# Kernel optimization log

Hardware: AMD Instinct MI355X
Metric: run time of the kernel (lower is better)

The kernel has to match this reference:

```python
import jax, jax.numpy as jnp
import numpy as np


def setup_inputs() -> dict:
    key = jax.random.key(0)
    k1, k2 = jax.random.split(key)
    K, D = 8192, 256
    z_e_x = jax.random.normal(k1, (4, D, 32, 64), dtype=jnp.float32)
    # matches uniform(-1/K, 1/K) init scale-wise, but any values work for correctness
    codebook = jax.random.uniform(k2, (K, D), dtype=jnp.float32, minval=-1.0 / K, maxval=1.0 / K)
    return {"z_e_x": z_e_x, "codebook": codebook}


def reference(z_e_x, codebook):
    b, D, h, t = z_e_x.shape
    K = codebook.shape[0]
    # permute to channels-last and flatten: [b*h*t, D]
    x = jnp.transpose(z_e_x, (0, 2, 3, 1)).reshape(-1, D)
    x_sqr = jnp.sum(x * x, axis=1, keepdims=True)          # [N, 1]
    c_sqr = jnp.sum(codebook * codebook, axis=1)           # [K]
    distances = x_sqr + c_sqr - 2.0 * jnp.einsum('nd,kd->nk', x, codebook)
    indices = jnp.argmin(distances, axis=1)                # [N] int
    # gather quantized codes and restore [b, D, h, t] layout
    z_q_x_bar = jnp.transpose(codebook[indices].reshape(b, h, t, D), (0, 3, 1, 2))
    # commitment loss: 0.25 * mse(z_e_x, stop_grad(z_q_x_bar))
    commitment_loss = 0.25 * jnp.mean((z_e_x - jax.lax.stop_gradient(z_q_x_bar)) ** 2)
    return indices.reshape(b, h, t), z_q_x_bar, commitment_loss
```

## Files before the change

kernel.cpp:

```cpp
#include <hip/hip_runtime.h>
#include <hip/hip_bf16.h>
#include <cstdint>
#include <cstddef>


#define NPTS 8192
#define KCB  8192

typedef __attribute__((ext_vector_type(4))) float f32x4;

#define X_OFF    0u
#define XB8_OFF  8388608u
#define CB8_OFF  10485760u
#define CSQ_OFF  12582912u
#define XSQP_OFF 12615680u
#define CNT_OFF  12877824u
#define CAND_OFF 12910592u
#define PART_OFF 15007744u

__device__ __forceinline__ void gld_lds16(const void* g, void* l) {
  __builtin_amdgcn_global_load_lds(
      (const __attribute__((address_space(1))) void*)g,
      (__attribute__((address_space(3))) void*)l, 16, 0, 0);
}

__global__ __launch_bounds__(256) void prep_k(
    const float* __restrict__ z, const float* __restrict__ cb,
    float* __restrict__ x, unsigned char* __restrict__ xb8,
    unsigned char* __restrict__ cb8, float* __restrict__ csq,
    float* __restrict__ xsqp, unsigned int* __restrict__ cnt) {
  int blk = blockIdx.x;
  int tid = threadIdx.x;
  if (blk < 2048) {
    __shared__ float tile[32][33];
    int mb = blk & 63, db = (blk >> 6) & 7, b = blk >> 9;
    int m0 = mb * 32, d0 = db * 32;
    int tx = tid & 31, ty = tid >> 5;
    const float* inb = z + (size_t)b * 524288;
    #pragma unroll
    for (int j = 0; j < 4; ++j)
      tile[ty + j*8][tx] = inb[(size_t)(d0 + ty + j*8) * 2048 + m0 + tx];
    __syncthreads();
    int mm = tid >> 3, dg = tid & 7;
    float v0 = tile[dg*4+0][mm], v1 = tile[dg*4+1][mm];
    float v2 = tile[dg*4+2][mm], v3 = tile[dg*4+3][mm];
    int n = b * 2048 + m0 + mm;
    float4 f4 = {v0, v1, v2, v3};
    *(float4*)&x[(size_t)n * 256 + d0 + dg * 4] = f4;
    unsigned int pk = __builtin_amdgcn_cvt_pk_fp8_f32(v0, v1, 0, 0);
    pk = __builtin_amdgcn_cvt_pk_fp8_f32(v2, v3, pk, 1);
    *(unsigned int*)&xb8[(size_t)n * 256 + d0 + dg * 4] = pk;
    float s = v0*v0 + v1*v1 + v2*v2 + v3*v3;
    s += __shfl_xor(s, 1); s += __shfl_xor(s, 2); s += __shfl_xor(s, 4);
    if (dg == 0) xsqp[db * 8192 + n] = s;
  } else {
    int blk2 = blk - 2048;
    int wave = tid >> 6, lane = tid & 63;
    int row = blk2 * 4 + wave;
    float4 v = *(const float4*)&cb[(size_t)row * 256 + lane * 4];
    unsigned int pk = __builtin_amdgcn_cvt_pk_fp8_f32(v.x * 8192.f, v.y * 8192.f, 0, 0);
    pk = __builtin_amdgcn_cvt_pk_fp8_f32(v.z * 8192.f, v.w * 8192.f, pk, 1);
    *(unsigned int*)&cb8[(size_t)row * 256 + lane * 4] = pk;
    float s = v.x*v.x + v.y*v.y + v.z*v.z + v.w*v.w;
    #pragma unroll
    for (int off = 32; off > 0; off >>= 1) s += __shfl_xor(s, off);
    if (lane == 0) csq[row] = s;
    if (tid < 4) cnt[blk2 * 4 + tid] = 0u;
  }
}

__global__ __launch_bounds__(256, 4) void gemm_filter_k(
    const unsigned char* __restrict__ xb8, const unsigned char* __restrict__ cb8,
    const float* __restrict__ xsqp, unsigned int* __restrict__ cnt,
    int* __restrict__ cand) {
  __shared__ unsigned char smemB[4][2][4096];
  __shared__ int cand_s[64][20];
  __shared__ int ccnt_s[64];
  __shared__ float thr_s[64];
  const int tid = threadIdx.x;
  const int lane = tid & 63, w = tid >> 6;
  const int wn = w >> 1, wk = w & 1;
  const int half = lane >> 4;
  const int qr   = lane & 15;
  const int n0 = blockIdx.x * 64;
  const int kbase = blockIdx.y * 1024 + wk * 512;

  if (tid < 64) {
    float xs = 0.f;
    #pragma unroll
    for (int db = 0; db < 8; ++db) xs += xsqp[db * 8192 + n0 + tid];
    thr_s[tid] = 1.6455f * sqrtf(xs);
    ccnt_s[tid] = 0;
  }
  __syncthreads();

  long long a[2][8];
  #pragma unroll
  for (int i = 0; i < 2; ++i) {
    int arow = n0 + wn * 32 + i * 16 + qr;
    #pragma unroll
    for (int ds = 0; ds < 8; ++ds)
      a[i][ds] = *(const long long*)&xb8[(size_t)arow * 256 + ds * 32 + half * 8];
  }
  float thv[2][4], thmin[2];
  #pragma unroll
  for (int i = 0; i < 2; ++i) {
    #pragma unroll
    for (int r = 0; r < 4; ++r)
      thv[i][r] = thr_s[wn * 32 + i * 16 + half * 4 + r];
    thmin[i] = fminf(fminf(thv[i][0], thv[i][1]), fminf(thv[i][2], thv[i][3]));
  }
  asm volatile("s_waitcnt vmcnt(0)" ::: "memory");

#define STAGE_B(p_, cc_) do {                                                  \
    _Pragma("unroll")                                                          \
    for (int q = 0; q < 4; ++q) {                                              \
      int cw_ = q * 4 + (lane >> 4);                  \
      int src_ = ((2 * (lane & 15)) ^ (cw_ << 1)) * 8;                         \
      gld_lds16(&cb8[(size_t)(kbase + (cc_) * 16 + cw_) * 256 + src_],         \
                &smemB[w][p_][q * 1024]);                                      \
    }                                                                          \
  } while (0)

#define FOLD(av_, i_, kv_) do {                                                \
    float mx_ = fmaxf(fmaxf(av_[0], av_[1]), fmaxf(av_[2], av_[3]));           \
    if (mx_ > thmin[i_]) {                                                     \
      _Pragma("unroll")                                                        \
      for (int r = 0; r < 4; ++r) {                                            \
        if (av_[r] > thv[i_][r]) {                                             \
          int rloc_ = wn * 32 + (i_) * 16 + half * 4 + r;                      \
          int pos_ = atomicAdd(&ccnt_s[rloc_], 1);                             \
          if (pos_ < 20) cand_s[rloc_][pos_] = (kv_);                          \
        }                                                                      \
      }                                                                        \
    }                                                                          \
  } while (0)

#define ITER(cc_, p_, vm_) do {                                                \
    asm volatile("s_waitcnt vmcnt(" #vm_ ")" ::: "memory");                    \
    __builtin_amdgcn_sched_barrier(0);                                         \
    __builtin_amdgcn_s_setprio(1);                                             \
    f32x4 acc0 = zz, acc1 = zz;                                                \
    _Pragma("unroll")                                                          \
    for (int ds = 0; ds < 8; ++ds) {                                           \
      long long b = *(const long long*)                                        \
          &smemB[w][p_][qr * 256 + (((ds * 4 + half) ^ (qr << 1))) * 8];       \
      acc0 = __builtin_amdgcn_mfma_f32_16x16x32_fp8_fp8(a[0][ds], b, acc0, 0, 0, 0); \
      acc1 = __builtin_amdgcn_mfma_f32_16x16x32_fp8_fp8(a[1][ds], b, acc1, 0, 0, 0); \
    }                                                                          \
    __builtin_amdgcn_s_setprio(0);                                             \
    asm volatile("s_waitcnt lgkmcnt(0)" ::: "memory");     \
    if ((cc_) + 2 < 32) STAGE_B(p_, (cc_) + 2);                                \
    int kv = kbase + (cc_) * 16 + qr;                                          \
    FOLD(acc0, 0, kv); FOLD(acc1, 1, kv);                                      \
  } while (0)

  const f32x4 zz = {0.f, 0.f, 0.f, 0.f};
  STAGE_B(0, 0);
  STAGE_B(1, 1);
  #pragma unroll 1
  for (int c = 0; c < 30; c += 2) {
    ITER(c, 0, 4);
    ITER(c + 1, 1, 4);
  }
  ITER(30, 0, 4);
  ITER(31, 1, 0);
#undef STAGE_B
#undef ITER
#undef FOLD

  __syncthreads();
  if (tid < 64) {
    int local = ccnt_s[tid];
    int stored = local < 20 ? local : 20;
    unsigned int add = (unsigned int)stored + (local > 20 ? 0x100000u : 0u);
    unsigned int base = atomicAdd(&cnt[n0 + tid], add);
    for (int i2 = 0; i2 < stored; ++i2) {
      unsigned int p = base + (unsigned int)i2;
      if (p < 64u) cand[(size_t)(n0 + tid) * 64 + p] = cand_s[tid][i2];
    }
  }
}

__global__ __launch_bounds__(256) void rescore_k(
    const float* __restrict__ x, const float* __restrict__ cb,
    const float* __restrict__ csq, const float* __restrict__ xsqp,
    const unsigned int* __restrict__ cnt, const int* __restrict__ cand,
    float* __restrict__ outIdx) {
  __shared__ float xrow[256];
  __shared__ float sv[16];
  __shared__ int sk[16];
  __shared__ float xs_sh;
  int n = blockIdx.x, tid = threadIdx.x;
  int g = tid >> 4, l = tid & 15;
  if (tid == 0) {
    float s = 0.f;
    #pragma unroll
    for (int db = 0; db < 8; ++db) s += xsqp[db * 8192 + n];
    xs_sh = s;
  }
  xrow[tid] = x[(size_t)n * 256 + tid];
  __syncthreads();
  unsigned int raw = cnt[n];
  bool fb = (raw == 0u) || (raw > 64u);
  int M = fb ? KCB : (int)raw;
  float xs = xs_sh;
  float bs = 3.4e38f; int bk = 0x7fffffff;
  for (int c = g; c < M; c += 16) {
    int k = fb ? c : cand[n * 64 + c];
    const float* cr = cb + (size_t)k * 256;
    float dot = 0.f;
    #pragma unroll
    for (int j = 0; j < 16; ++j) dot = fmaf(xrow[j * 16 + l], cr[j * 16 + l], dot);
    #pragma unroll
    for (int off = 1; off < 16; off <<= 1) dot += __shfl_xor(dot, off);
    float s = (xs + csq[k]) - 2.0f * dot;
    if (s < bs || (s == bs && k < bk)) { bs = s; bk = k; }
  }
  if (l == 0) { sv[g] = bs; sk[g] = bk; }
  __syncthreads();
  if (tid == 0) {
    #pragma unroll
    for (int u = 1; u < 16; ++u)
      if (sv[u] < bs || (sv[u] == bs && sk[u] < bk)) { bs = sv[u]; bk = sk[u]; }
    outIdx[n] = (float)bk;
  }
}

__global__ void gather_k(const float* __restrict__ zin, const float* __restrict__ cb,
                         const float* __restrict__ outIdx, float* __restrict__ zq,
                         float* __restrict__ part) {
  __shared__ float red[256];
  int tid = threadIdx.x;
  int g = (blockIdx.x * 256 + tid) * 4;
  int b = g >> 19;
  int rem = g & 524287;
  int d = rem >> 11;
  int m = rem & 2047;
  int nb = b * 2048 + m;
  float4 z4 = *(const float4*)&zin[g];
  float4 i4 = *(const float4*)&outIdx[nb];
  float za[4] = {z4.x, z4.y, z4.z, z4.w};
  float ia[4] = {i4.x, i4.y, i4.z, i4.w};
  float4 c4;
  float* ca = (float*)&c4;
  float s = 0.f;
  #pragma unroll
  for (int u = 0; u < 4; ++u) {
    int idx = (int)ia[u];
    float c = cb[(size_t)idx * 256 + d];
    ca[u] = c;
    float diff = za[u] - c;
    s += diff * diff;
  }
  *(float4*)&zq[g] = c4;
  red[tid] = s;
  __syncthreads();
  for (int s2 = 128; s2 > 0; s2 >>= 1) {
    if (tid < s2) red[tid] += red[tid + s2];
    __syncthreads();
  }
  if (tid == 0) part[blockIdx.x] = red[0];
}

__global__ void loss_k(const float* __restrict__ part, float* __restrict__ outLoss) {
  __shared__ float red[256];
  int tid = threadIdx.x;
  float s = 0.f;
  for (int r = 0; r < 8; ++r) s += part[tid + r * 256];
  red[tid] = s;
  __syncthreads();
  for (int s2 = 128; s2 > 0; s2 >>= 1) {
    if (tid < s2) red[tid] += red[tid + s2];
    __syncthreads();
  }
  if (tid == 0) outLoss[0] = 0.25f * red[0] / 2097152.0f;
}

extern "C" void kernel_launch(void* const* d_in, const int* in_sizes, int n_in,
                              void* d_out, int out_size, void* d_ws, size_t ws_size,
                              hipStream_t stream) {
  const float* z  = (const float*)d_in[0];
  const float* cb = (const float*)d_in[1];
  float* out = (float*)d_out;
  char* ws = (char*)d_ws;
  float* x            = (float*)(ws + X_OFF);
  unsigned char* xb8  = (unsigned char*)(ws + XB8_OFF);
  unsigned char* cb8  = (unsigned char*)(ws + CB8_OFF);
  float* csq          = (float*)(ws + CSQ_OFF);
  float* xsqp         = (float*)(ws + XSQP_OFF);
  unsigned int* cnt   = (unsigned int*)(ws + CNT_OFF);
  int* cand           = (int*)(ws + CAND_OFF);
  float* part         = (float*)(ws + PART_OFF);

  prep_k<<<4096, 256, 0, stream>>>(z, cb, x, xb8, cb8, csq, xsqp, cnt);
  gemm_filter_k<<<dim3(128, 8), 256, 0, stream>>>(xb8, cb8, xsqp, cnt, cand);
  rescore_k<<<NPTS, 256, 0, stream>>>(x, cb, csq, xsqp, cnt, cand, out);
  gather_k<<<2048, 256, 0, stream>>>(z, cb, out, out + 8192, part);
  loss_k<<<1, 256, 0, stream>>>(part, out + 8192 + 2097152);
}
```

Baseline: 82.09 us.

## Load codebook tiles directly into registers with a pre-permuted fp8 layout

After: 112.7 us. 1.37x slower.

```diff
diff --git a/kernel.cpp b/kernel.cpp
--- a/kernel.cpp
+++ b/kernel.cpp
@@ -8,6 +8,7 @@
 #define KCB  8192
 
 typedef __attribute__((ext_vector_type(4))) float f32x4;
+typedef __attribute__((ext_vector_type(2))) long long ll2;
 
 #define X_OFF    0u
 #define XB8_OFF  8388608u
@@ -17,12 +18,6 @@
 #define CNT_OFF  12877824u
 #define CAND_OFF 12910592u
 #define PART_OFF 15007744u
-
-__device__ __forceinline__ void gld_lds16(const void* g, void* l) {
-  __builtin_amdgcn_global_load_lds(
-      (const __attribute__((address_space(1))) void*)g,
-      (__attribute__((address_space(3))) void*)l, 16, 0, 0);
-}
 
 __global__ __launch_bounds__(256) void prep_k(
     const float* __restrict__ z, const float* __restrict__ cb,
@@ -60,7 +55,9 @@
     float4 v = *(const float4*)&cb[(size_t)row * 256 + lane * 4];
     unsigned int pk = __builtin_amdgcn_cvt_pk_fp8_f32(v.x * 8192.f, v.y * 8192.f, 0, 0);
     pk = __builtin_amdgcn_cvt_pk_fp8_f32(v.z * 8192.f, v.w * 8192.f, pk, 1);
-    *(unsigned int*)&cb8[(size_t)row * 256 + lane * 4] = pk;
+    int d0 = lane * 4;
+    int ds = d0 >> 5, hf = (d0 >> 3) & 3, bo = d0 & 7;
+    *(unsigned int*)&cb8[(size_t)row * 256 + hf * 64 + ds * 8 + bo] = pk;
     float s = v.x*v.x + v.y*v.y + v.z*v.z + v.w*v.w;
     #pragma unroll
     for (int off = 32; off > 0; off >>= 1) s += __shfl_xor(s, off);
@@ -73,7 +70,6 @@
     const unsigned char* __restrict__ xb8, const unsigned char* __restrict__ cb8,
     const float* __restrict__ xsqp, unsigned int* __restrict__ cnt,
     int* __restrict__ cand) {
-  __shared__ unsigned char smemB[4][2][4096];
   __shared__ int cand_s[64][20];
   __shared__ int ccnt_s[64];
   __shared__ float thr_s[64];
@@ -110,16 +106,14 @@
       thv[i][r] = thr_s[wn * 32 + i * 16 + half * 4 + r];
     thmin[i] = fminf(fminf(thv[i][0], thv[i][1]), fminf(thv[i][2], thv[i][3]));
   }
-  asm volatile("s_waitcnt vmcnt(0)" ::: "memory");
-
-#define STAGE_B(p_, cc_) do {                                                  \
-    _Pragma("unroll")                                                          \
-    for (int q = 0; q < 4; ++q) {                                              \
-      int cw_ = q * 4 + (lane >> 4);                  \
-      int src_ = ((2 * (lane & 15)) ^ (cw_ << 1)) * 8;                         \
-      gld_lds16(&cb8[(size_t)(kbase + (cc_) * 16 + cw_) * 256 + src_],         \
-                &smemB[w][p_][q * 1024]);                                      \
-    }                                                                          \
+
+#define LOADB(n0_, n1_, n2_, n3_, cc_) do {                                    \
+    const unsigned char* s_ =                                                  \
+        &cb8[(size_t)(kbase + (cc_) * 16 + qr) * 256 + half * 64];             \
+    n0_ = *(const ll2*)(s_);                                                   \
+    n1_ = *(const ll2*)(s_ + 16);                                              \
+    n2_ = *(const ll2*)(s_ + 32);                                              \
+    n3_ = *(const ll2*)(s_ + 48);                                              \
   } while (0)
 
 #define FOLD(av_, i_, kv_) do {                                                \
@@ -136,37 +130,46 @@
     }                                                                          \
   } while (0)
 
-#define ITER(cc_, p_, vm_) do {                                                \
-    asm volatile("s_waitcnt vmcnt(" #vm_ ")" ::: "memory");                    \
-    __builtin_amdgcn_sched_barrier(0);                                         \
+#define MFMA_FOLD(n0_, n1_, n2_, n3_, cc_) do {                                \
     __builtin_amdgcn_s_setprio(1);                                             \
     f32x4 acc0 = zz, acc1 = zz;                                                \
-    _Pragma("unroll")                                                          \
-    for (int ds = 0; ds < 8; ++ds) {                                           \
-      long long b = *(const long long*)                                        \
-          &smemB[w][p_][qr * 256 + (((ds * 4 + half) ^ (qr << 1))) * 8];       \
-      acc0 = __builtin_amdgcn_mfma_f32_16x16x32_fp8_fp8(a[0][ds], b, acc0, 0, 0, 0); \
-      acc1 = __builtin_amdgcn_mfma_f32_16x16x32_fp8_fp8(a[1][ds], b, acc1, 0, 0, 0); \
-    }                                                                          \
+    acc0 = __builtin_amdgcn_mfma_f32_16x16x32_fp8_fp8(a[0][0], n0_.x, acc0, 0, 0, 0); \
+    acc1 = __builtin_amdgcn_mfma_f32_16x16x32_fp8_fp8(a[1][0], n0_.x, acc1, 0, 0, 0); \
+    acc0 = __builtin_amdgcn_mfma_f32_16x16x32_fp8_fp8(a[0][1], n0_.y, acc0, 0, 0, 0); \
+    acc1 = __builtin_amdgcn_mfma_f32_16x16x32_fp8_fp8(a[1][1], n0_.y, acc1, 0, 0, 0); \
+    acc0 = __builtin_amdgcn_mfma_f32_16x16x32_fp8_fp8(a[0][2], n1_.x, acc0, 0, 0, 0); \
+    acc1 = __builtin_amdgcn_mfma_f32_16x16x32_fp8_fp8(a[1][2], n1_.x, acc1, 0, 0, 0); \
+    acc0 = __builtin_amdgcn_mfma_f32_16x16x32_fp8_fp8(a[0][3], n1_.y, acc0, 0, 0, 0); \
+    acc1 = __builtin_amdgcn_mfma_f32_16x16x32_fp8_fp8(a[1][3], n1_.y, acc1, 0, 0, 0); \
+    acc0 = __builtin_amdgcn_mfma_f32_16x16x32_fp8_fp8(a[0][4], n2_.x, acc0, 0, 0, 0); \
+    acc1 = __builtin_amdgcn_mfma_f32_16x16x32_fp8_fp8(a[1][4], n2_.x, acc1, 0, 0, 0); \
+    acc0 = __builtin_amdgcn_mfma_f32_16x16x32_fp8_fp8(a[0][5], n2_.y, acc0, 0, 0, 0); \
+    acc1 = __builtin_amdgcn_mfma_f32_16x16x32_fp8_fp8(a[1][5], n2_.y, acc1, 0, 0, 0); \
+    acc0 = __builtin_amdgcn_mfma_f32_16x16x32_fp8_fp8(a[0][6], n3_.x, acc0, 0, 0, 0); \
+    acc1 = __builtin_amdgcn_mfma_f32_16x16x32_fp8_fp8(a[1][6], n3_.x, acc1, 0, 0, 0); \
+    acc0 = __builtin_amdgcn_mfma_f32_16x16x32_fp8_fp8(a[0][7], n3_.y, acc0, 0, 0, 0); \
+    acc1 = __builtin_amdgcn_mfma_f32_16x16x32_fp8_fp8(a[1][7], n3_.y, acc1, 0, 0, 0); \
     __builtin_amdgcn_s_setprio(0);                                             \
-    asm volatile("s_waitcnt lgkmcnt(0)" ::: "memory");     \
-    if ((cc_) + 2 < 32) STAGE_B(p_, (cc_) + 2);                                \
     int kv = kbase + (cc_) * 16 + qr;                                          \
     FOLD(acc0, 0, kv); FOLD(acc1, 1, kv);                                      \
   } while (0)
 
   const f32x4 zz = {0.f, 0.f, 0.f, 0.f};
-  STAGE_B(0, 0);
-  STAGE_B(1, 1);
+  ll2 p0, p1, p2, p3, q0, q1, q2, q3;
+
+  LOADB(p0, p1, p2, p3, 0);
   #pragma unroll 1
   for (int c = 0; c < 30; c += 2) {
-    ITER(c, 0, 4);
-    ITER(c + 1, 1, 4);
-  }
-  ITER(30, 0, 4);
-  ITER(31, 1, 0);
-#undef STAGE_B
-#undef ITER
+    LOADB(q0, q1, q2, q3, c + 1);
+    MFMA_FOLD(p0, p1, p2, p3, c);
+    LOADB(p0, p1, p2, p3, c + 2);
+    MFMA_FOLD(q0, q1, q2, q3, c + 1);
+  }
+  LOADB(q0, q1, q2, q3, 31);
+  MFMA_FOLD(p0, p1, p2, p3, 30);
+  MFMA_FOLD(q0, q1, q2, q3, 31);
+#undef LOADB
+#undef MFMA_FOLD
 #undef FOLD
 
   __syncthreads();
```
